# Optimization experiments

Measured on AMD Instinct MI355X. Metric: run time of the kernel, lower is better.

Reference implementation:

```python
import jax, jax.numpy as jnp
import numpy as np

B, T, D_MODEL, HEADS = 2, 2048, 1024, 16
D_HEAD = D_MODEL // HEADS


def setup_inputs() -> dict:
    key = jax.random.key(0)
    ks = jax.random.split(key, 9)
    s = 1.0 / np.sqrt(D_HEAD)
    return {
        "x": jax.random.normal(ks[0], (B, T, D_MODEL), dtype=jnp.float32),
        "Wq": jax.random.normal(ks[1], (D_HEAD, D_HEAD), dtype=jnp.float32) * s,
        "bq": jax.random.normal(ks[2], (D_HEAD,), dtype=jnp.float32) * 0.01,
        "Wk": jax.random.normal(ks[3], (D_HEAD, D_HEAD), dtype=jnp.float32) * s,
        "bk": jax.random.normal(ks[4], (D_HEAD,), dtype=jnp.float32) * 0.01,
        "Wv": jax.random.normal(ks[5], (D_HEAD, D_HEAD), dtype=jnp.float32) * s,
        "bv": jax.random.normal(ks[6], (D_HEAD,), dtype=jnp.float32) * 0.01,
        "Wp": jax.random.normal(ks[7], (D_MODEL, D_MODEL), dtype=jnp.float32) * (1.0 / np.sqrt(D_MODEL)),
        "bp": jax.random.normal(ks[8], (D_MODEL,), dtype=jnp.float32) * 0.01,
    }


def reference(x, Wq, bq, Wk, bk, Wv, bv, Wp, bp):
    b, t, c = x.shape
    xh = x.reshape(b, t, HEADS, D_HEAD)  # [B,T,H,dh]
    # per-head linear projections (weights shared across heads), nn.Linear: y = x @ W.T + b
    q = jnp.einsum('bthd,ed->bhte', xh, Wq) + bq  # [B,H,T,dh]
    k = jnp.einsum('bthd,ed->bhte', xh, Wk) + bk
    v = jnp.einsum('bthd,ed->bhte', xh, Wv) + bv
    # NOTE: original scales by sqrt(C) = sqrt(d_model), not sqrt(d_head)
    scale = 1.0 / jnp.sqrt(jnp.float32(c))
    att = jnp.einsum('bhqd,bhkd->bhqk', q, k) * scale  # [B,H,T,T]
    att = jax.nn.softmax(att, axis=-1)
    out = jnp.einsum('bhqk,bhkd->bhqd', att, v)  # [B,H,T,dh]
    out = out.transpose(0, 2, 1, 3).reshape(b, t, c)  # [B,T,C]
    out = out @ Wp.T + bp
    return out
```

## Files before the change

kernel.cpp:

```cpp
#include <hip/hip_runtime.h>
#include <hip/hip_bf16.h>

#define B_ 2
#define T_ 2048
#define DM_ 1024
#define H_ 16
#define DH_ 64
#define QSCALE 0.045084220027780106f

typedef unsigned short u16;
typedef unsigned int u32;
typedef __attribute__((ext_vector_type(2))) unsigned int u32x2;
typedef __attribute__((ext_vector_type(4))) unsigned int u32x4;
typedef __attribute__((ext_vector_type(4))) float f32x4v;
typedef __attribute__((ext_vector_type(8))) short bf16x8;
typedef __attribute__((ext_vector_type(4))) float f32x4;

__device__ __forceinline__ u16 f2bf(float f) {
    u32 u = __float_as_uint(f);
    return (u16)((u + 0x7FFF + ((u >> 16) & 1)) >> 16);
}
__device__ __forceinline__ float bf2f(u16 h) {
    return __uint_as_float(((u32)h) << 16);
}
__device__ __forceinline__ float exp2_fast(float x) {
    float r;
    asm("v_exp_f32 %0, %1" : "=v"(r) : "v"(x));
    return r;
}
__device__ __forceinline__ u32 cvtpk_bf16(float lo, float hi) {
    u32 r;
    asm("v_cvt_pk_bf16_f32 %0, %1, %2" : "=v"(r) : "v"(lo), "v"(hi));
    return r;
}

__device__ __forceinline__ const bf16x8* frag_at(const u16* base, int row, int c16) {
    return (const bf16x8*)((const char*)base + row * 128 + ((c16 ^ (row & 7)) << 4));
}

__global__ __launch_bounds__(256) void wsplit_all(
    const float* __restrict__ Wq, const float* __restrict__ Wk,
    const float* __restrict__ Wv, const float* __restrict__ Wp,
    u16* __restrict__ W6, u16* __restrict__ Wh, u16* __restrict__ Wl)
{
    const int i = blockIdx.x * 256 + threadIdx.x;
    if (i < DM_ * DM_) {
        const float w = Wp[i];
        const u16 hi = f2bf(w);
        Wh[i] = hi;
        Wl[i] = f2bf(w - bf2f(hi));
    } else {
        const int j = i - DM_ * DM_;
        const int mat = j >> 12, idx = j & 4095;
        const float w = (mat == 0) ? Wq[idx] : (mat == 1) ? Wk[idx] : Wv[idx];
        const u16 hi = f2bf(w);
        W6[(mat * 2) * 4096 + idx] = hi;
        W6[(mat * 2 + 1) * 4096 + idx] = f2bf(w - bf2f(hi));
    }
}

__global__ __launch_bounds__(256) void qkv_mfma(
    const float* __restrict__ x,
    const float* __restrict__ bq, const float* __restrict__ bk,
    const float* __restrict__ bv, const u16* __restrict__ W6,
    u16* __restrict__ Q, u16* __restrict__ K, u16* __restrict__ VT)
{
    __shared__ u16 Ws[6 * 4096];

    const int tid = threadIdx.x;
    const int wid = tid >> 6;
    const int lane = tid & 63;
    const int li = lane & 15, g = lane >> 4;

    const int bh = blockIdx.x >> 4;
    const int t0 = (blockIdx.x & 15) * 128;
    const int b = bh >> 4, h = bh & 15;
    const int tw0 = t0 + wid * 32;

    #pragma unroll
    for (int j = 0; j < 12; ++j) {
        const int gi = j * 256 + tid;
        const int tile = gi >> 9;
        const int t16 = gi & 511;
        const int r = t16 >> 3, c16 = t16 & 7;
        const int c16s = c16 ^ (r & 7);
        __builtin_amdgcn_global_load_lds(
            (const __attribute__((address_space(1))) u32*)((const char*)W6 + tile * 8192 + r * 128 + (c16s << 4)),
            (__attribute__((address_space(3))) u32*)((char*)Ws + gi * 16),
            16, 0, 0);
    }

    const float* xb = x + ((size_t)b * T_) * DM_ + h * 64;
    f32x4v xr[2][2][2];
    #pragma unroll
    for (int mt = 0; mt < 2; ++mt)
        #pragma unroll
        for (int kt = 0; kt < 2; ++kt) {
            const float* p = xb + (size_t)(tw0 + 16 * mt + li) * DM_ + kt * 32 + g * 8;
            xr[mt][kt][0] = *(const f32x4v*)p;
            xr[mt][kt][1] = *(const f32x4v*)(p + 4);
        }

    float bq_r[4], bk_r[4], bv_r[4][4];
    #pragma unroll
    for (int nt = 0; nt < 4; ++nt) { bq_r[nt] = bq[16 * nt + li]; bk_r[nt] = bk[16 * nt + li]; }
    #pragma unroll
    for (int vd = 0; vd < 4; ++vd)
        #pragma unroll
        for (int rg = 0; rg < 4; ++rg) bv_r[vd][rg] = bv[16 * vd + 4 * g + rg];

    __syncthreads();

    bf16x8 xhf[2][2], xlf[2][2];
    #pragma unroll
    for (int mt = 0; mt < 2; ++mt)
        #pragma unroll
        for (int kt = 0; kt < 2; ++kt) {
            u32 hw[4], lw[4];
            #pragma unroll
            for (int q2 = 0; q2 < 2; ++q2) {
                const f32x4v v = xr[mt][kt][q2];
                const u32 p0 = cvtpk_bf16(v[0], v[1]);
                const u32 p1 = cvtpk_bf16(v[2], v[3]);
                const float l0 = v[0] - __uint_as_float(p0 << 16);
                const float l1 = v[1] - __uint_as_float(p0 & 0xFFFF0000u);
                const float l2 = v[2] - __uint_as_float(p1 << 16);
                const float l3 = v[3] - __uint_as_float(p1 & 0xFFFF0000u);
                hw[q2 * 2] = p0; hw[q2 * 2 + 1] = p1;
                lw[q2 * 2] = cvtpk_bf16(l0, l1);
                lw[q2 * 2 + 1] = cvtpk_bf16(l2, l3);
            }
            xhf[mt][kt] = *(const bf16x8*)hw;
            xlf[mt][kt] = *(const bf16x8*)lw;
        }

    const u16* Wqh = Ws;
    const u16* Wql = Ws + 4096;
    const u16* Wkh = Ws + 8192;
    const u16* Wkl = Ws + 12288;
    const u16* Wvh = Ws + 16384;
    const u16* Wvl = Ws + 20480;

    const size_t qk_base = ((size_t)bh * T_) * DH_;

    {
        f32x4 acc[2][4];
        #pragma unroll
        for (int mt = 0; mt < 2; ++mt)
            #pragma unroll
            for (int nt = 0; nt < 4; ++nt) acc[mt][nt] = (f32x4){0.f, 0.f, 0.f, 0.f};
        #pragma unroll
        for (int nt = 0; nt < 4; ++nt)
            #pragma unroll
            for (int kt = 0; kt < 2; ++kt) {
                const bf16x8 wh = *frag_at(Wqh, 16 * nt + li, 4 * kt + g);
                const bf16x8 wl = *frag_at(Wql, 16 * nt + li, 4 * kt + g);
                #pragma unroll
                for (int mt = 0; mt < 2; ++mt) {
                    acc[mt][nt] = __builtin_amdgcn_mfma_f32_16x16x32_bf16(xhf[mt][kt], wh, acc[mt][nt], 0, 0, 0);
                    acc[mt][nt] = __builtin_amdgcn_mfma_f32_16x16x32_bf16(xlf[mt][kt], wh, acc[mt][nt], 0, 0, 0);
                    acc[mt][nt] = __builtin_amdgcn_mfma_f32_16x16x32_bf16(xhf[mt][kt], wl, acc[mt][nt], 0, 0, 0);
                }
            }
        #pragma unroll
        for (int mt = 0; mt < 2; ++mt)
            #pragma unroll
            for (int rg = 0; rg < 4; ++rg) {
                const int t = tw0 + 16 * mt + 4 * g + rg;
                #pragma unroll
                for (int nt = 0; nt < 4; ++nt)
                    Q[qk_base + (size_t)t * DH_ + 16 * nt + li] =
                        f2bf((acc[mt][nt][rg] + bq_r[nt]) * QSCALE);
            }
    }

    {
        f32x4 acc[2][4];
        #pragma unroll
        for (int mt = 0; mt < 2; ++mt)
            #pragma unroll
            for (int nt = 0; nt < 4; ++nt) acc[mt][nt] = (f32x4){0.f, 0.f, 0.f, 0.f};
        #pragma unroll
        for (int nt = 0; nt < 4; ++nt)
            #pragma unroll
            for (int kt = 0; kt < 2; ++kt) {
                const bf16x8 wh = *frag_at(Wkh, 16 * nt + li, 4 * kt + g);
                const bf16x8 wl = *frag_at(Wkl, 16 * nt + li, 4 * kt + g);
                #pragma unroll
                for (int mt = 0; mt < 2; ++mt) {
                    acc[mt][nt] = __builtin_amdgcn_mfma_f32_16x16x32_bf16(xhf[mt][kt], wh, acc[mt][nt], 0, 0, 0);
                    acc[mt][nt] = __builtin_amdgcn_mfma_f32_16x16x32_bf16(xlf[mt][kt], wh, acc[mt][nt], 0, 0, 0);
                    acc[mt][nt] = __builtin_amdgcn_mfma_f32_16x16x32_bf16(xhf[mt][kt], wl, acc[mt][nt], 0, 0, 0);
                }
            }
        #pragma unroll
        for (int mt = 0; mt < 2; ++mt)
            #pragma unroll
            for (int rg = 0; rg < 4; ++rg) {
                const int t = tw0 + 16 * mt + 4 * g + rg;
                #pragma unroll
                for (int nt = 0; nt < 4; ++nt)
                    K[qk_base + (size_t)t * DH_ + 16 * nt + li] =
                        f2bf(acc[mt][nt][rg] + bk_r[nt]);
            }
    }

    {
        f32x4 acc[4][2];
        #pragma unroll
        for (int vd = 0; vd < 4; ++vd)
            #pragma unroll
            for (int tc = 0; tc < 2; ++tc) acc[vd][tc] = (f32x4){0.f, 0.f, 0.f, 0.f};
        #pragma unroll
        for (int vd = 0; vd < 4; ++vd)
            #pragma unroll
            for (int kt = 0; kt < 2; ++kt) {
                const bf16x8 ah = *frag_at(Wvh, 16 * vd + li, 4 * kt + g);
                const bf16x8 al = *frag_at(Wvl, 16 * vd + li, 4 * kt + g);
                #pragma unroll
                for (int tc = 0; tc < 2; ++tc) {
                    acc[vd][tc] = __builtin_amdgcn_mfma_f32_16x16x32_bf16(ah, xhf[tc][kt], acc[vd][tc], 0, 0, 0);
                    acc[vd][tc] = __builtin_amdgcn_mfma_f32_16x16x32_bf16(al, xhf[tc][kt], acc[vd][tc], 0, 0, 0);
                    acc[vd][tc] = __builtin_amdgcn_mfma_f32_16x16x32_bf16(ah, xlf[tc][kt], acc[vd][tc], 0, 0, 0);
                }
            }
        u16* VTb = VT + (size_t)bh * DH_ * T_;
        #pragma unroll
        for (int vd = 0; vd < 4; ++vd)
            #pragma unroll
            for (int rg = 0; rg < 4; ++rg) {
                const int d = 16 * vd + 4 * g + rg;
                #pragma unroll
                for (int tc = 0; tc < 2; ++tc)
                    VTb[(size_t)d * T_ + tw0 + 16 * tc + li] =
                        f2bf(acc[vd][tc][rg] + bv_r[vd][rg]);
            }
    }
}

__global__ __launch_bounds__(512) void attn_mfma(
    const u16* __restrict__ Q, const u16* __restrict__ K,
    const u16* __restrict__ VT, u16* __restrict__ Ah, u16* __restrict__ Al)
{
    __shared__ char smem[49152];

    const int tid = threadIdx.x;
    const int wid = tid >> 6;
    const int lane = tid & 63;
    const int li = lane & 15, g = lane >> 4;
    const int flat = blockIdx.x;
    const int bh = (flat & 7) + ((flat >> 7) << 3);
    const int qx = (flat >> 3) & 15;
    const int q0 = qx * 128 + wid * 16;

    const size_t bhoff = (size_t)bh * T_ * DH_;

    bf16x8 qf[2];
    {
        const u16* Qp = Q + bhoff + (size_t)q0 * DH_;
        #pragma unroll
        for (int kt = 0; kt < 2; ++kt)
            qf[kt] = *(const bf16x8*)(Qp + li * DH_ + kt * 32 + g * 8);
    }

    f32x4 o[4];
    float l_part = 0.f;
    #pragma unroll
    for (int dt = 0; dt < 4; ++dt) o[dt] = (f32x4){0.f, 0.f, 0.f, 0.f};

    const int swk = li & 7;
    const char* ldsA[2];
    #pragma unroll
    for (int kt = 0; kt < 2; ++kt)
        ldsA[kt] = smem + li * 128 + (((4 * kt + g) ^ swk) << 4);
    const char* ldsPr[2];
    #pragma unroll
    for (int kt = 0; kt < 2; ++kt)
        ldsPr[kt] = smem + 32768 + wid * 2048 + li * 128 + (((4 * kt + g) ^ swk) << 4);
    char* ldsPw[4];
    #pragma unroll
    for (int ct = 0; ct < 4; ++ct)
        ldsPw[ct] = smem + 32768 + wid * 2048 + li * 128 + ((32 * ct + 8 * g) ^ (swk << 4));

    const int sl_r = lane >> 3;
    const int sl_c = (lane & 7) ^ sl_r;
    const char* kgp = (const char*)(K + bhoff) + wid * 1024 + sl_r * 128 + (sl_c << 4);
    const char* vgp = (const char*)(VT + (size_t)bh * DH_ * T_) + wid * (8 * T_ * 2) + sl_r * (T_ * 2) + (sl_c << 4);

#define STAGE(BUF)                                                                      \
    {                                                                                   \
        __builtin_amdgcn_global_load_lds(                                               \
            (const __attribute__((address_space(1))) u32*)kgp,                          \
            (__attribute__((address_space(3))) u32*)(smem + (BUF) + wid * 1024),        \
            16, 0, 0);                                                                  \
        __builtin_amdgcn_global_load_lds(                                               \
            (const __attribute__((address_space(1))) u32*)vgp,                          \
            (__attribute__((address_space(3))) u32*)(smem + 16384 + (BUF) + wid * 1024),\
            16, 0, 0);                                                                  \
        kgp += 8192; vgp += 128;                                                        \
    }

#define ATTN_ITER(BUF, PREFBUF, DO_PREF)                                                \
    {                                                                                   \
        __syncthreads();                                                                \
        if (DO_PREF) STAGE(PREFBUF);                                                    \
        f32x4 s[4];                                                                     \
        _Pragma("unroll")                                                               \
        for (int ct = 0; ct < 4; ++ct) s[ct] = (f32x4){0.f, 0.f, 0.f, 0.f};             \
        __builtin_amdgcn_s_setprio(1);                                                  \
        _Pragma("unroll")                                                               \
        for (int ct = 0; ct < 4; ++ct) {                                                \
            _Pragma("unroll")                                                           \
            for (int kt = 0; kt < 2; ++kt) {                                            \
                const bf16x8 kf = *(const bf16x8*)(ldsA[kt] + (BUF) + 2048 * ct);       \
                s[ct] = __builtin_amdgcn_mfma_f32_16x16x32_bf16(kf, qf[kt], s[ct], 0, 0, 0); \
            }                                                                           \
        }                                                                               \
        __builtin_amdgcn_s_setprio(0);                                                  \
        float lacc = 0.f;                                                               \
        _Pragma("unroll")                                                               \
        for (int ct = 0; ct < 4; ++ct) {                                                \
            const float p0 = exp2_fast(s[ct][0]);                                       \
            const float p1 = exp2_fast(s[ct][1]);                                       \
            const float p2 = exp2_fast(s[ct][2]);                                       \
            const float p3 = exp2_fast(s[ct][3]);                                       \
            lacc += (p0 + p1) + (p2 + p3);                                              \
            u32x2 w;                                                                    \
            w.x = cvtpk_bf16(p0, p1);                                                   \
            w.y = cvtpk_bf16(p2, p3);                                                   \
            *(u32x2*)ldsPw[ct] = w;                                                     \
        }                                                                               \
        l_part += lacc;                                                                 \
        __builtin_amdgcn_s_setprio(1);                                                  \
        _Pragma("unroll")                                                               \
        for (int kt = 0; kt < 2; ++kt) {                                                \
            const bf16x8 pf = *(const bf16x8*)ldsPr[kt];                                \
            _Pragma("unroll")                                                           \
            for (int dt = 0; dt < 4; ++dt) {                                            \
                const bf16x8 vf = *(const bf16x8*)(ldsA[kt] + 16384 + (BUF) + 2048 * dt); \
                o[dt] = __builtin_amdgcn_mfma_f32_16x16x32_bf16(vf, pf, o[dt], 0, 0, 0); \
            }                                                                           \
        }                                                                               \
        __builtin_amdgcn_s_setprio(0);                                                  \
    }

    STAGE(0);
    for (int kv = 0; kv < T_ / 64; kv += 2) {
        ATTN_ITER(0, 8192, true);
        ATTN_ITER(8192, 0, (kv + 2 < T_ / 64));
    }
#undef ATTN_ITER
#undef STAGE

    float lt = l_part;
    lt += __shfl_xor(lt, 16);
    lt += __shfl_xor(lt, 32);
    const float inv = 1.0f / lt;

    __syncthreads();

    char* ehi = smem + wid * 4096;
    char* elo = ehi + 2048;
    #pragma unroll
    for (int dt = 0; dt < 4; ++dt) {
        const float v0 = o[dt][0] * inv;
        const float v1 = o[dt][1] * inv;
        const float v2 = o[dt][2] * inv;
        const float v3 = o[dt][3] * inv;
        u32x2 wh, wl;
        wh.x = cvtpk_bf16(v0, v1);
        wh.y = cvtpk_bf16(v2, v3);
        const float l0 = v0 - __uint_as_float(wh.x << 16);
        const float l1 = v1 - __uint_as_float(wh.x & 0xFFFF0000u);
        const float l2 = v2 - __uint_as_float(wh.y << 16);
        const float l3 = v3 - __uint_as_float(wh.y & 0xFFFF0000u);
        wl.x = cvtpk_bf16(l0, l1);
        wl.y = cvtpk_bf16(l2, l3);
        const int byteoff = li * 128 + ((32 * dt + 8 * g) ^ (swk << 4));
        *(u32x2*)(ehi + byteoff) = wh;
        *(u32x2*)(elo + byteoff) = wl;
    }

    const int b = bh >> 4, h = bh & 15;
    const int sub = lane & 7;
    const int row8 = lane >> 3;
    #pragma unroll
    for (int rr = 0; rr < 2; ++rr) {
        const int row = 8 * rr + row8;
        const int byteoff = row * 128 + ((sub ^ row8) << 4);
        const size_t gidx = ((size_t)b * T_ + q0 + row) * DM_ + h * 64 + sub * 8;
        *(u32x4*)(Ah + gidx) = *(const u32x4*)(ehi + byteoff);
        *(u32x4*)(Al + gidx) = *(const u32x4*)(elo + byteoff);
    }
}

__global__ __launch_bounds__(512) void proj_mfma(
    const u16* __restrict__ Ah, const u16* __restrict__ Al,
    const u16* __restrict__ Wh, const u16* __restrict__ Wl,
    const float* __restrict__ bp, float* __restrict__ out)
{
    __shared__ char smem[131072];

    const int tid = threadIdx.x;
    const int wid = tid >> 6;
    const int lane = tid & 63;
    const int li = lane & 15, g = lane >> 4;
    const int row0 = blockIdx.y * 128, col0 = blockIdx.x * 128;

    const int mat = wid >> 1, half = wid & 1;
    const char* gsrc;
    if (mat == 0)      gsrc = (const char*)(Ah + (size_t)row0 * DM_);
    else if (mat == 1) gsrc = (const char*)(Al + (size_t)row0 * DM_);
    else if (mat == 2) gsrc = (const char*)(Wh + (size_t)col0 * DM_);
    else               gsrc = (const char*)(Wl + (size_t)col0 * DM_);
    const int r_local = half * 64 + (lane >> 3);
    const int c16s = (lane & 7) ^ (lane >> 3);
    const char* gp0 = gsrc + (size_t)r_local * (DM_ * 2) + (c16s << 4);
    const int ldst0 = mat * 16384 + half * 8192;

#define PSTAGE(BUF, STEP)                                                                \
    {                                                                                    \
        _Pragma("unroll")                                                                \
        for (int j = 0; j < 8; ++j) {                                                    \
            __builtin_amdgcn_global_load_lds(                                            \
                (const __attribute__((address_space(1))) u32*)(gp0 + (size_t)(STEP) * 128 + (size_t)j * (8 * DM_ * 2)), \
                (__attribute__((address_space(3))) u32*)(smem + (BUF) + ldst0 + j * 1024),\
                16, 0, 0);                                                               \
        }                                                                                \
    }

    const int wr = wid >> 1, wc = wid & 1;

    f32x4 acc[2][4];
    #pragma unroll
    for (int m = 0; m < 2; ++m)
        #pragma unroll
        for (int n = 0; n < 4; ++n) acc[m][n] = (f32x4){0.f, 0.f, 0.f, 0.f};

    PSTAGE(0, 0);
    for (int step = 0; step < 16; ++step) {
        const int buf = (step & 1) * 65536;
        __syncthreads();
        if (step < 15) PSTAGE(buf ^ 65536, step + 1);

        const u16* pAh = (const u16*)(smem + buf);
        const u16* pAl = (const u16*)(smem + buf + 16384);
        const u16* pWh = (const u16*)(smem + buf + 32768);
        const u16* pWl = (const u16*)(smem + buf + 49152);

        __builtin_amdgcn_s_setprio(1);
        #pragma unroll
        for (int kt = 0; kt < 2; ++kt) {
            bf16x8 ah[2], al[2], wh[4], wl[4];
            #pragma unroll
            for (int m = 0; m < 2; ++m) {
                ah[m] = *frag_at(pAh, wr * 32 + m * 16 + li, kt * 4 + g);
                al[m] = *frag_at(pAl, wr * 32 + m * 16 + li, kt * 4 + g);
            }
            #pragma unroll
            for (int n = 0; n < 4; ++n) {
                wh[n] = *frag_at(pWh, wc * 64 + n * 16 + li, kt * 4 + g);
                wl[n] = *frag_at(pWl, wc * 64 + n * 16 + li, kt * 4 + g);
            }
            #pragma unroll
            for (int m = 0; m < 2; ++m)
                #pragma unroll
                for (int n = 0; n < 4; ++n) {
                    acc[m][n] = __builtin_amdgcn_mfma_f32_16x16x32_bf16(ah[m], wh[n], acc[m][n], 0, 0, 0);
                    acc[m][n] = __builtin_amdgcn_mfma_f32_16x16x32_bf16(al[m], wh[n], acc[m][n], 0, 0, 0);
                    acc[m][n] = __builtin_amdgcn_mfma_f32_16x16x32_bf16(ah[m], wl[n], acc[m][n], 0, 0, 0);
                }
        }
        __builtin_amdgcn_s_setprio(0);
    }
#undef PSTAGE

    const int orow = row0 + wr * 32;
    const int ocol = col0 + wc * 64;
    float bias[4];
    #pragma unroll
    for (int n = 0; n < 4; ++n) bias[n] = bp[ocol + n * 16 + li];
    #pragma unroll
    for (int m = 0; m < 2; ++m)
        #pragma unroll
        for (int n = 0; n < 4; ++n)
            #pragma unroll
            for (int q = 0; q < 4; ++q)
                out[(size_t)(orow + m * 16 + g * 4 + q) * DM_ + ocol + n * 16 + li] =
                    acc[m][n][q] + bias[n];
}

extern "C" void kernel_launch(void* const* d_in, const int* in_sizes, int n_in,
                              void* d_out, int out_size, void* d_ws, size_t ws_size,
                              hipStream_t stream) {
    const float* x  = (const float*)d_in[0];
    const float* Wq = (const float*)d_in[1];
    const float* bq = (const float*)d_in[2];
    const float* Wk = (const float*)d_in[3];
    const float* bk = (const float*)d_in[4];
    const float* Wv = (const float*)d_in[5];
    const float* bv = (const float*)d_in[6];
    const float* Wp = (const float*)d_in[7];
    const float* bp = (const float*)d_in[8];
    float* out = (float*)d_out;

    const size_t n_qkv = (size_t)B_ * H_ * T_ * DH_;
    const size_t n_w   = (size_t)DM_ * DM_;
    u16* Qb  = (u16*)d_ws;
    u16* Kb  = Qb + n_qkv;
    u16* VTb = Kb + n_qkv;
    u16* Ahb = VTb + n_qkv;
    u16* Alb = Ahb + n_qkv;
    u16* Whb = Alb + n_qkv;
    u16* Wlb = Whb + n_w;
    u16* W6b = Wlb + n_w;

    wsplit_all<<<(n_w + 12288) / 256, 256, 0, stream>>>(Wq, Wk, Wv, Wp, W6b, Whb, Wlb);
    qkv_mfma<<<32 * 16, 256, 0, stream>>>(x, bq, bk, bv, W6b, Qb, Kb, VTb);
    attn_mfma<<<512, 512, 0, stream>>>(Qb, Kb, VTb, Ahb, Alb);
    proj_mfma<<<dim3(DM_ / 128, (B_ * T_) / 128), 512, 0, stream>>>(Ahb, Alb, Whb, Wlb, bp, out);
}
```

Before: 90.39 us.

## Switch attention to 32x32x16 MFMA with in-register P via permlane swap

Rewrites the attention kernel to use 32x32x16 bf16 MFMA tiles, with 4 waves each handling 32 query rows instead of 8 waves of 16. The probability matrix P is repacked in registers with v_permlane32_swap and fed straight into the PV MFMA, so the LDS round-trip for P goes away. Shared memory drops to 32KB and blocks to 256 threads. The aim is fewer LDS accesses and less instruction overhead per FLOP, at the cost of more accumulator registers per wave and fewer waves per block.

Result: no change. 91.27 us (+1.0%).

```diff
diff --git a/kernel.cpp b/kernel.cpp
--- a/kernel.cpp
+++ b/kernel.cpp
@@ -15,6 +15,7 @@
 typedef __attribute__((ext_vector_type(4))) float f32x4v;
 typedef __attribute__((ext_vector_type(8))) short bf16x8;
 typedef __attribute__((ext_vector_type(4))) float f32x4;
+typedef __attribute__((ext_vector_type(16))) float f32x16;
 
 __device__ __forceinline__ u16 f2bf(float f) {
     u32 u = __float_as_uint(f);
@@ -238,157 +239,162 @@
     }
 }
 
-__global__ __launch_bounds__(512) void attn_mfma(
+__global__ __launch_bounds__(256) void attn_mfma(
     const u16* __restrict__ Q, const u16* __restrict__ K,
     const u16* __restrict__ VT, u16* __restrict__ Ah, u16* __restrict__ Al)
 {
-    __shared__ char smem[49152];
+    __shared__ char smem[32768];
 
     const int tid = threadIdx.x;
     const int wid = tid >> 6;
     const int lane = tid & 63;
-    const int li = lane & 15, g = lane >> 4;
+    const int l = lane & 31, h = lane >> 5;
     const int flat = blockIdx.x;
     const int bh = (flat & 7) + ((flat >> 7) << 3);
     const int qx = (flat >> 3) & 15;
-    const int q0 = qx * 128 + wid * 16;
+    const int q0 = qx * 128 + wid * 32;
 
     const size_t bhoff = (size_t)bh * T_ * DH_;
 
-    bf16x8 qf[2];
+    bf16x8 qf[4];
     {
-        const u16* Qp = Q + bhoff + (size_t)q0 * DH_;
-        #pragma unroll
-        for (int kt = 0; kt < 2; ++kt)
-            qf[kt] = *(const bf16x8*)(Qp + li * DH_ + kt * 32 + g * 8);
-    }
-
-    f32x4 o[4];
+        const u16* Qp = Q + bhoff + (size_t)(q0 + l) * DH_ + 8 * h;
+        #pragma unroll
+        for (int kt = 0; kt < 4; ++kt)
+            qf[kt] = *(const bf16x8*)(Qp + 16 * kt);
+    }
+
+    f32x16 o0 = {}, o1 = {};
     float l_part = 0.f;
-    #pragma unroll
-    for (int dt = 0; dt < 4; ++dt) o[dt] = (f32x4){0.f, 0.f, 0.f, 0.f};
-
-    const int swk = li & 7;
-    const char* ldsA[2];
-    #pragma unroll
-    for (int kt = 0; kt < 2; ++kt)
-        ldsA[kt] = smem + li * 128 + (((4 * kt + g) ^ swk) << 4);
-    const char* ldsPr[2];
-    #pragma unroll
-    for (int kt = 0; kt < 2; ++kt)
-        ldsPr[kt] = smem + 32768 + wid * 2048 + li * 128 + (((4 * kt + g) ^ swk) << 4);
-    char* ldsPw[4];
-    #pragma unroll
-    for (int ct = 0; ct < 4; ++ct)
-        ldsPw[ct] = smem + 32768 + wid * 2048 + li * 128 + ((32 * ct + 8 * g) ^ (swk << 4));
+
+    const char* ldsR[4];
+    #pragma unroll
+    for (int kt = 0; kt < 4; ++kt)
+        ldsR[kt] = smem + l * 128 + ((((2 * kt + h) ^ (l & 7))) << 4);
 
     const int sl_r = lane >> 3;
     const int sl_c = (lane & 7) ^ sl_r;
-    const char* kgp = (const char*)(K + bhoff) + wid * 1024 + sl_r * 128 + (sl_c << 4);
-    const char* vgp = (const char*)(VT + (size_t)bh * DH_ * T_) + wid * (8 * T_ * 2) + sl_r * (T_ * 2) + (sl_c << 4);
-
-#define STAGE(BUF)                                                                      \
-    {                                                                                   \
-        __builtin_amdgcn_global_load_lds(                                               \
-            (const __attribute__((address_space(1))) u32*)kgp,                          \
-            (__attribute__((address_space(3))) u32*)(smem + (BUF) + wid * 1024),        \
-            16, 0, 0);                                                                  \
-        __builtin_amdgcn_global_load_lds(                                               \
-            (const __attribute__((address_space(1))) u32*)vgp,                          \
-            (__attribute__((address_space(3))) u32*)(smem + 16384 + (BUF) + wid * 1024),\
-            16, 0, 0);                                                                  \
-        kgp += 8192; vgp += 128;                                                        \
-    }
-
-#define ATTN_ITER(BUF, PREFBUF, DO_PREF)                                                \
-    {                                                                                   \
-        __syncthreads();                                                                \
-        if (DO_PREF) STAGE(PREFBUF);                                                    \
-        f32x4 s[4];                                                                     \
-        _Pragma("unroll")                                                               \
-        for (int ct = 0; ct < 4; ++ct) s[ct] = (f32x4){0.f, 0.f, 0.f, 0.f};             \
-        __builtin_amdgcn_s_setprio(1);                                                  \
-        _Pragma("unroll")                                                               \
-        for (int ct = 0; ct < 4; ++ct) {                                                \
-            _Pragma("unroll")                                                           \
-            for (int kt = 0; kt < 2; ++kt) {                                            \
-                const bf16x8 kf = *(const bf16x8*)(ldsA[kt] + (BUF) + 2048 * ct);       \
-                s[ct] = __builtin_amdgcn_mfma_f32_16x16x32_bf16(kf, qf[kt], s[ct], 0, 0, 0); \
-            }                                                                           \
-        }                                                                               \
-        __builtin_amdgcn_s_setprio(0);                                                  \
-        float lacc = 0.f;                                                               \
-        _Pragma("unroll")                                                               \
-        for (int ct = 0; ct < 4; ++ct) {                                                \
-            const float p0 = exp2_fast(s[ct][0]);                                       \
-            const float p1 = exp2_fast(s[ct][1]);                                       \
-            const float p2 = exp2_fast(s[ct][2]);                                       \
-            const float p3 = exp2_fast(s[ct][3]);                                       \
-            lacc += (p0 + p1) + (p2 + p3);                                              \
-            u32x2 w;                                                                    \
-            w.x = cvtpk_bf16(p0, p1);                                                   \
-            w.y = cvtpk_bf16(p2, p3);                                                   \
-            *(u32x2*)ldsPw[ct] = w;                                                     \
-        }                                                                               \
-        l_part += lacc;                                                                 \
-        __builtin_amdgcn_s_setprio(1);                                                  \
-        _Pragma("unroll")                                                               \
-        for (int kt = 0; kt < 2; ++kt) {                                                \
-            const bf16x8 pf = *(const bf16x8*)ldsPr[kt];                                \
-            _Pragma("unroll")                                                           \
-            for (int dt = 0; dt < 4; ++dt) {                                            \
-                const bf16x8 vf = *(const bf16x8*)(ldsA[kt] + 16384 + (BUF) + 2048 * dt); \
-                o[dt] = __builtin_amdgcn_mfma_f32_16x16x32_bf16(vf, pf, o[dt], 0, 0, 0); \
-            }                                                                           \
-        }                                                                               \
-        __builtin_amdgcn_s_setprio(0);                                                  \
+    const char* kgp0 = (const char*)(K + bhoff) + (16 * wid + sl_r) * 128 + (sl_c << 4);
+    const char* kgp1 = kgp0 + 8 * 128;
+    const char* vgp0 = (const char*)(VT + (size_t)bh * DH_ * T_) + (size_t)(16 * wid + sl_r) * (T_ * 2) + (sl_c << 4);
+    const char* vgp1 = vgp0 + (size_t)8 * (T_ * 2);
+    const int kdst = 16 * wid * 128 + lane * 16;
+
+#define STAGE(BUF)                                                                       \
+    {                                                                                    \
+        __builtin_amdgcn_global_load_lds(                                                \
+            (const __attribute__((address_space(1))) u32*)kgp0,                          \
+            (__attribute__((address_space(3))) u32*)(smem + (BUF) + kdst), 16, 0, 0);    \
+        __builtin_amdgcn_global_load_lds(                                                \
+            (const __attribute__((address_space(1))) u32*)kgp1,                          \
+            (__attribute__((address_space(3))) u32*)(smem + (BUF) + kdst + 1024), 16, 0, 0); \
+        __builtin_amdgcn_global_load_lds(                                                \
+            (const __attribute__((address_space(1))) u32*)vgp0,                          \
+            (__attribute__((address_space(3))) u32*)(smem + 16384 + (BUF) + kdst), 16, 0, 0); \
+        __builtin_amdgcn_global_load_lds(                                                \
+            (const __attribute__((address_space(1))) u32*)vgp1,                          \
+            (__attribute__((address_space(3))) u32*)(smem + 16384 + (BUF) + kdst + 1024), 16, 0, 0); \
+        kgp0 += 8192; kgp1 += 8192; vgp0 += 128; vgp1 += 128;                            \
+    }
+
+#define ATTN_ITER(BUF, DO_PREF)                                                          \
+    {                                                                                    \
+        __syncthreads();                                                                 \
+        if (DO_PREF) STAGE((BUF) ^ 8192);                                                \
+        f32x16 s0 = {}, s1 = {};                                                         \
+        __builtin_amdgcn_s_setprio(1);                                                   \
+        _Pragma("unroll")                                                                \
+        for (int kt = 0; kt < 4; ++kt) {                                                 \
+            const bf16x8 kf0 = *(const bf16x8*)(ldsR[kt] + (BUF));                       \
+            const bf16x8 kf1 = *(const bf16x8*)(ldsR[kt] + (BUF) + 4096);                \
+            s0 = __builtin_amdgcn_mfma_f32_32x32x16_bf16(kf0, qf[kt], s0, 0, 0, 0);      \
+            s1 = __builtin_amdgcn_mfma_f32_32x32x16_bf16(kf1, qf[kt], s1, 0, 0, 0);      \
+        }                                                                                \
+        __builtin_amdgcn_s_setprio(0);                                                   \
+        float lacc = 0.f;                                                                \
+        _Pragma("unroll")                                                                \
+        for (int r = 0; r < 16; ++r) { s0[r] = exp2_fast(s0[r]); lacc += s0[r]; }        \
+        _Pragma("unroll")                                                                \
+        for (int r = 0; r < 16; ++r) { s1[r] = exp2_fast(s1[r]); lacc += s1[r]; }        \
+        l_part += lacc;                                                                  \
+        __builtin_amdgcn_s_setprio(1);                                                   \
+        _Pragma("unroll")                                                                \
+        for (int kt = 0; kt < 4; ++kt) {                                                 \
+            const int rb = (kt & 1) * 8;                                                 \
+            u32 w0, w1, w2, w3;                                                          \
+            if (kt < 2) {                                                                \
+                w0 = cvtpk_bf16(s0[rb + 0], s0[rb + 1]);                                 \
+                w1 = cvtpk_bf16(s0[rb + 2], s0[rb + 3]);                                 \
+                w2 = cvtpk_bf16(s0[rb + 4], s0[rb + 5]);                                 \
+                w3 = cvtpk_bf16(s0[rb + 6], s0[rb + 7]);                                 \
+            } else {                                                                     \
+                w0 = cvtpk_bf16(s1[rb + 0], s1[rb + 1]);                                 \
+                w1 = cvtpk_bf16(s1[rb + 2], s1[rb + 3]);                                 \
+                w2 = cvtpk_bf16(s1[rb + 4], s1[rb + 5]);                                 \
+                w3 = cvtpk_bf16(s1[rb + 6], s1[rb + 7]);                                 \
+            }                                                                            \
+            asm("v_permlane32_swap_b32 %0, %1" : "+v"(w0), "+v"(w2));                    \
+            asm("v_permlane32_swap_b32 %0, %1" : "+v"(w1), "+v"(w3));                    \
+            u32x4 pw; pw[0] = w0; pw[1] = w1; pw[2] = w2; pw[3] = w3;                    \
+            const bf16x8 pf = __builtin_bit_cast(bf16x8, pw);                            \
+            const bf16x8 vf0 = *(const bf16x8*)(ldsR[kt] + 16384 + (BUF));               \
+            const bf16x8 vf1 = *(const bf16x8*)(ldsR[kt] + 16384 + (BUF) + 4096);        \
+            o0 = __builtin_amdgcn_mfma_f32_32x32x16_bf16(vf0, pf, o0, 0, 0, 0);          \
+            o1 = __builtin_amdgcn_mfma_f32_32x32x16_bf16(vf1, pf, o1, 0, 0, 0);          \
+        }                                                                                \
+        __builtin_amdgcn_s_setprio(0);                                                   \
     }
 
     STAGE(0);
-    for (int kv = 0; kv < T_ / 64; kv += 2) {
-        ATTN_ITER(0, 8192, true);
-        ATTN_ITER(8192, 0, (kv + 2 < T_ / 64));
+    for (int it = 0; it < 32; it += 2) {
+        ATTN_ITER(0, true);
+        ATTN_ITER(8192, (it + 2 < 32));
     }
 #undef ATTN_ITER
 #undef STAGE
 
-    float lt = l_part;
-    lt += __shfl_xor(lt, 16);
-    lt += __shfl_xor(lt, 32);
+    const float lt = l_part + __shfl_xor(l_part, 32);
     const float inv = 1.0f / lt;
 
     __syncthreads();
 
-    char* ehi = smem + wid * 4096;
-    char* elo = ehi + 2048;
-    #pragma unroll
-    for (int dt = 0; dt < 4; ++dt) {
-        const float v0 = o[dt][0] * inv;
-        const float v1 = o[dt][1] * inv;
-        const float v2 = o[dt][2] * inv;
-        const float v3 = o[dt][3] * inv;
-        u32x2 wh, wl;
-        wh.x = cvtpk_bf16(v0, v1);
-        wh.y = cvtpk_bf16(v2, v3);
-        const float l0 = v0 - __uint_as_float(wh.x << 16);
-        const float l1 = v1 - __uint_as_float(wh.x & 0xFFFF0000u);
-        const float l2 = v2 - __uint_as_float(wh.y << 16);
-        const float l3 = v3 - __uint_as_float(wh.y & 0xFFFF0000u);
-        wl.x = cvtpk_bf16(l0, l1);
-        wl.y = cvtpk_bf16(l2, l3);
-        const int byteoff = li * 128 + ((32 * dt + 8 * g) ^ (swk << 4));
-        *(u32x2*)(ehi + byteoff) = wh;
-        *(u32x2*)(elo + byteoff) = wl;
-    }
-
-    const int b = bh >> 4, h = bh & 15;
+    char* ehi = smem + wid * 8192;
+    char* elo = ehi + 4096;
+    #pragma unroll
+    for (int db = 0; db < 2; ++db) {
+        #pragma unroll
+        for (int rr = 0; rr < 4; ++rr) {
+            float v0, v1, v2, v3;
+            if (db == 0) {
+                v0 = o0[4 * rr + 0] * inv; v1 = o0[4 * rr + 1] * inv;
+                v2 = o0[4 * rr + 2] * inv; v3 = o0[4 * rr + 3] * inv;
+            } else {
+                v0 = o1[4 * rr + 0] * inv; v1 = o1[4 * rr + 1] * inv;
+                v2 = o1[4 * rr + 2] * inv; v3 = o1[4 * rr + 3] * inv;
+            }
+            u32x2 wh, wl;
+            wh.x = cvtpk_bf16(v0, v1);
+            wh.y = cvtpk_bf16(v2, v3);
+            const float r0 = v0 - __uint_as_float(wh.x << 16);
+            const float r1 = v1 - __uint_as_float(wh.x & 0xFFFF0000u);
+            const float r2 = v2 - __uint_as_float(wh.y << 16);
+            const float r3 = v3 - __uint_as_float(wh.y & 0xFFFF0000u);
+            wl.x = cvtpk_bf16(r0, r1);
+            wl.y = cvtpk_bf16(r2, r3);
+            const int byteoff = l * 128 + (((4 * db + rr) ^ (l & 7)) << 4) + 8 * h;
+            *(u32x2*)(ehi + byteoff) = wh;
+            *(u32x2*)(elo + byteoff) = wl;
+        }
+    }
+
+    const int b = bh >> 4, head = bh & 15;
     const int sub = lane & 7;
     const int row8 = lane >> 3;
     #pragma unroll
-    for (int rr = 0; rr < 2; ++rr) {
+    for (int rr = 0; rr < 4; ++rr) {
         const int row = 8 * rr + row8;
         const int byteoff = row * 128 + ((sub ^ row8) << 4);
-        const size_t gidx = ((size_t)b * T_ + q0 + row) * DM_ + h * 64 + sub * 8;
+        const size_t gidx = ((size_t)b * T_ + q0 + row) * DM_ + head * 64 + sub * 8;
         *(u32x4*)(Ah + gidx) = *(const u32x4*)(ehi + byteoff);
         *(u32x4*)(Al + gidx) = *(const u32x4*)(elo + byteoff);
     }
@@ -517,6 +523,6 @@
 
     wsplit_all<<<(n_w + 12288) / 256, 256, 0, stream>>>(Wq, Wk, Wv, Wp, W6b, Whb, Wlb);
     qkv_mfma<<<32 * 16, 256, 0, stream>>>(x, bq, bk, bv, W6b, Qb, Kb, VTb);
-    attn_mfma<<<512, 512, 0, stream>>>(Qb, Kb, VTb, Ahb, Alb);
+    attn_mfma<<<512, 256, 0, stream>>>(Qb, Kb, VTb, Ahb, Alb);
     proj_mfma<<<dim3(DM_ / 128, (B_ * T_) / 128), 512, 0, stream>>>(Ahb, Alb, Whb, Wlb, bp, out);
 }
```
